# Kernel tuning notes

Hardware: AMD Instinct MI355X
Metric: run time of the kernel (lower is better)

## Reference

```python
import jax, jax.numpy as jnp
import numpy as np

N_NODES = 38000   # 19 feature types x ~2000 categories
IN_DIM = 64
HID = 128         # hid_num in source
R = 8             # number of relations
E = 200000        # edges per relation
N_ROWS = 60000    # data rows
F = 19            # len(features)
N_CLASSES = 10


def setup_inputs() -> dict:
    key = jax.random.key(0)
    ks = jax.random.split(key, 20)
    s_in = 1.0 / np.sqrt(IN_DIM)
    s_h = 1.0 / np.sqrt(HID)
    inp = {
        "node_feats": jax.random.normal(ks[0], (N_NODES, IN_DIM), jnp.float32),
        "edges_src": jax.random.randint(ks[1], (R, E), 0, N_NODES),
        "edges_dst": jax.random.randint(ks[2], (R, E), 0, N_NODES),
        "row_idx": jax.random.randint(ks[3], (N_ROWS, F), 0, N_NODES),
        "row_mask": jax.random.randint(ks[4], (N_ROWS, F), 0, 2).astype(bool),
        # input linear
        "W_in": jax.random.normal(ks[5], (IN_DIM, HID), jnp.float32) * s_in,
        "b_in": jnp.zeros((HID,), jnp.float32),
        # RGCN layer 1 and 2: per-relation GraphConv weights
        "W1": jax.random.normal(ks[6], (R, HID, HID), jnp.float32) * s_h,
        "b1": jnp.zeros((R, HID), jnp.float32),
        "W2": jax.random.normal(ks[7], (R, HID, HID), jnp.float32) * s_h,
        "b2": jnp.zeros((R, HID), jnp.float32),
        # MLP head
        "Wm1": jax.random.normal(ks[8], (HID, HID), jnp.float32) * s_h,
        "bm1": jnp.zeros((HID,), jnp.float32),
        "Wm2": jax.random.normal(ks[9], (HID, HID), jnp.float32) * s_h,
        "bm2": jnp.zeros((HID,), jnp.float32),
        "Wm3": jax.random.normal(ks[10], (HID, N_CLASSES), jnp.float32) * s_h,
        "bm3": jnp.zeros((N_CLASSES,), jnp.float32),
    }
    return inp


def _hetero_conv(h, src, dst, W, b):
    """DGL HeteroGraphConv(sum) of GraphConv(norm='both') over R relations."""
    n = h.shape[0]
    out = jnp.zeros((n, W.shape[2]), h.dtype)
    ones = jnp.ones((src.shape[1],), h.dtype)
    for r in range(src.shape[0]):
        deg_out = jax.ops.segment_sum(ones, src[r], num_segments=n)
        deg_in = jax.ops.segment_sum(ones, dst[r], num_segments=n)
        norm_s = jnp.where(deg_out > 0, deg_out, 1.0) ** -0.5
        norm_d = jnp.where(deg_in > 0, deg_in, 1.0) ** -0.5
        msg = h[src[r]] * norm_s[src[r], None]            # [E, hid]
        agg = jax.ops.segment_sum(msg, dst[r], num_segments=n)
        out = out + (agg * norm_d[:, None]) @ W[r] + b[r]
    return out


def reference(node_feats, edges_src, edges_dst, row_idx, row_mask,
              W_in, b_in, W1, b1, W2, b2, Wm1, bm1, Wm2, bm2, Wm3, bm3):
    # input linear + relu (applied to every node type's features)
    h = jax.nn.relu(node_feats @ W_in + b_in)            # [N_nodes, HID]
    # 2-layer RGCN
    h = jax.nn.relu(_hetero_conv(h, edges_src, edges_dst, W1, b1))
    h = _hetero_conv(h, edges_src, edges_dst, W2, b2)    # [N_nodes, HID]
    # vectorized ragged gather + masked mean (replaces per-row python loop)
    m = row_mask.astype(h.dtype)                          # [N_rows, F]
    emb = h[row_idx] * m[..., None]                       # [N_rows, F, HID]
    cnt = jnp.maximum(m.sum(-1, keepdims=True), 1.0)
    mean_feat = emb.sum(1) / cnt                          # [N_rows, HID]
    # MLP head
    x = jax.nn.relu(mean_feat @ Wm1 + bm1)
    x = jax.nn.relu(x @ Wm2 + bm2)
    return x @ Wm3 + bm3                                  # [N_rows, N_CLASSES]
```

## Files before the change

### kernel.cpp

```cpp
#include <hip/hip_runtime.h>
#include <hip/hip_bf16.h>

#define NN    38000
#define HID   128
#define RR    8
#define EE    200000
#define NROWS 60000
#define FF    19
#define NCLS  10
#define NRD   (RR*NN)
#define HB    38912
#define CH    16
#define CE    (EE/CH)
#define NSEG  19

typedef __hip_bfloat16 bf16;
typedef __attribute__((ext_vector_type(8))) short short8;
typedef __attribute__((ext_vector_type(4))) float floatx4;
typedef __attribute__((ext_vector_type(2))) float float2v;

__device__ __forceinline__ float b2f(bf16 x){ return __bfloat162float(x); }
__device__ __forceinline__ bf16  f2b(float x){ return __float2bfloat16(x); }

__device__ __forceinline__ int geti(const void* a, long long i, int wide){
  return wide ? (int)(((const long long*)a)[i]) : ((const int*)a)[i];
}

__global__ void k_fill(float* out, int n, float v){
  int i = blockIdx.x*256 + threadIdx.x;
  if (i < n) out[i] = v;
}

__global__ void k_sniff(const void* mask, const void* ridx, const void* esrc, int* flags){
  int lane = threadIdx.x;
  const unsigned short* mu = (const unsigned short*)mask;
  int l3f80e=0, l3f80o=0, lbytehi=0, loddnz=0, lother=0;
  for (int i = lane; i < 4096; i += 64){
    unsigned v = mu[i];
    if (v == 0) continue;
    if (v == 0x3F80){ if (i & 1) l3f80o = 1; else l3f80e = 1; continue; }
    unsigned lo = v & 0xFF, hi = v >> 8;
    int lob = (lo == 0 || lo == 1 || lo == 0xFF);
    int hib = (hi == 0 || hi == 1 || hi == 0xFF);
    if (lob && hib){ if (hi) lbytehi = 1; if (i & 1) loddnz = 1; continue; }
    lother = 1;
  }
  int a3f80e = __any(l3f80e);
  int a3f80o = __any(l3f80o);
  int abytehi = __any(lbytehi);
  int aoddnz = __any(loddnz);
  int aother = __any(lother);
  int mtype = -1;
  if (!aother){
    if (a3f80e && !abytehi && !aoddnz)       mtype = 2;
    else if (a3f80o && !a3f80e && !abytehi)  mtype = 3;
    else if (!a3f80e && !a3f80o){
      if (abytehi || aoddnz) mtype = 1;
      else                   mtype = 0;
    }
  }
  const int* es = (const int*)esrc;
  int loddE = 0, lseenE = 0;
  for (int i = lane; i < 512; i += 64){
    if (es[2*i+1] != 0) loddE = 1;
    if (es[2*i] > 1)    lseenE = 1;
  }
  int fE = (!__any(loddE) && __any(lseenE)) ? 1 : 0;
  const int* ri = (const int*)ridx;
  int loddI = 0, lseenI = 0;
  for (int i = lane; i < 512; i += 64){
    if (ri[2*i+1] != 0) loddI = 1;
    if (ri[2*i] > 1)    lseenI = 1;
  }
  int fI = (!__any(loddI) && __any(lseenI)) ? 1 : 0;
  if (lane == 0){ flags[1] = mtype; flags[3] = fE; flags[4] = fI; }
}


__global__ __launch_bounds__(1024) void kg_hist(const void* esrc, const void* edst,
                                                unsigned short* __restrict__ ghd,
                                                unsigned short* __restrict__ ghs,
                                                const int* flags){
  __shared__ int hist[HB];
  int t = threadIdx.x;
  for (int i = t; i < HB; i += 1024) hist[i] = 0;
  __syncthreads();
  int b = blockIdx.x;
  int side = b >> 7;
  int r = (b >> 4) & 7, c = b & 15;
  int wide = flags[3];
  const void* e = side ? esrc : edst;
  long long base = (long long)r*EE + (long long)c*CE;
  if (!wide){
    const int* p = (const int*)e + base;
    for (int i = t; i < CE; i += 1024) atomicAdd(&hist[p[i]], 1);
  } else {
    const long long* p = (const long long*)e + base;
    for (int i = t; i < CE; i += 1024) atomicAdd(&hist[(int)p[i]], 1);
  }
  __syncthreads();
  unsigned short* out = (side ? ghs : ghd) + (long long)(r*CH + c)*HB;
  for (int i = t; i < HB; i += 1024) out[i] = (unsigned short)hist[i];
}

__global__ void kg_tot(const unsigned short* __restrict__ ghd,
                       const unsigned short* __restrict__ ghs,
                       int* __restrict__ totg, float* __restrict__ ns){
  int i = blockIdx.x*256 + threadIdx.x;
  if (i >= RR*HB) return;
  int r = i / HB, bin = i - r*HB;
  int sd = 0, ss = 0;
#pragma unroll
  for (int c = 0; c < CH; c++){
    sd += ghd[(long long)(r*CH+c)*HB + bin];
    ss += ghs[(long long)(r*CH+c)*HB + bin];
  }
  totg[i] = sd;
  if (bin < NN) ns[r*NN + bin] = rsqrtf((float)(ss > 0 ? ss : 1));
}

__global__ __launch_bounds__(1024) void kg_scanA(const int* __restrict__ totg,
                                                 int* __restrict__ rowptr,
                                                 int* __restrict__ segsum){
  __shared__ int wsum[16];
  int b = blockIdx.x;
  int r = b / NSEG, seg = b - r*NSEG;
  int t = threadIdx.x;
  int base = seg*2048;
  int v0 = totg[r*HB + base + 2*t];
  int v1 = totg[r*HB + base + 2*t + 1];
  int s = v0 + v1;
  int lane = t & 63, w = t >> 6;
  int sc = s;
  for (int off = 1; off < 64; off <<= 1){
    int u = __shfl_up(sc, off);
    if (lane >= off) sc += u;
  }
  if (lane == 63) wsum[w] = sc;
  __syncthreads();
  if (t < 16){
    int v = wsum[t];
    int scw = v;
    for (int off = 1; off < 16; off <<= 1){
      int u = __shfl_up(scw, off);
      if (t >= off) scw += u;
    }
    wsum[t] = scw - v;
  }
  __syncthreads();
  int ex = (sc - s) + wsum[w];
  int bin0 = base + 2*t;
  if (bin0 < NN)     rowptr[r*NN + bin0]     = ex;
  if (bin0 + 1 < NN) rowptr[r*NN + bin0 + 1] = ex + v0;
  if (t == 1023) segsum[b] = ex + s;
}

__global__ void kg_scanB(const int* __restrict__ segsum, int* __restrict__ segoff){
  int r = threadIdx.x;
  if (r < RR){
    int acc = r*EE;
    for (int s = 0; s < NSEG; s++){
      int v = segsum[r*NSEG + s];
      segoff[r*NSEG + s] = acc;
      acc += v;
    }
  }
}

__global__ void kg_curs(const unsigned short* __restrict__ ghd,
                        int* __restrict__ rowptr,
                        const int* __restrict__ segoff,
                        int* __restrict__ gcurs){
  int i = blockIdx.x*256 + threadIdx.x;
  if (i >= NRD) return;
  int r = i / NN, bin = i - r*NN;
  int p = rowptr[i] + segoff[r*NSEG + (bin >> 11)];
  rowptr[i] = p;
  if (i == 0) rowptr[NRD] = RR*EE;
#pragma unroll
  for (int c = 0; c < CH; c++){
    gcurs[(long long)(r*CH+c)*HB + bin] = p;
    p += ghd[(long long)(r*CH+c)*HB + bin];
  }
}

__global__ __launch_bounds__(1024) void kg_scatter(const void* esrc, const void* edst,
                                                   const int* __restrict__ gcurs,
                                                   const float* __restrict__ ns,
                                                   int2* __restrict__ csrw, const int* flags){
  __shared__ int cur[HB];
  int t = threadIdx.x, b = blockIdx.x;
  int r = b >> 4, c = b & 15;
  const int* g = gcurs + (long long)(r*CH + c)*HB;
  for (int i = t; i < HB; i += 1024) cur[i] = g[i];
  __syncthreads();
  if (b == 0 && t < 8){ int2 z; z.x = 0; z.y = 0; csrw[RR*EE + t] = z; }
  int wide = flags[3];
  const float* nsr = ns + r*NN;
  long long base = (long long)r*EE + (long long)c*CE;
  if (!wide){
    const int* ps = (const int*)esrc + base;
    const int* pd = (const int*)edst + base;
    for (int i = t; i < CE; i += 1024){
      int d = pd[i], s = ps[i];
      int pos = atomicAdd(&cur[d], 1);
      int2 v; v.x = s << 6; v.y = __float_as_int(nsr[s]);
      csrw[pos] = v;
    }
  } else {
    const long long* ps = (const long long*)esrc + base;
    const long long* pd = (const long long*)edst + base;
    for (int i = t; i < CE; i += 1024){
      int d = (int)pd[i], s = (int)ps[i];
      int pos = atomicAdd(&cur[d], 1);
      int2 v; v.x = s << 6; v.y = __float_as_int(nsr[s]);
      csrw[pos] = v;
    }
  }
}


__global__ void k_packall(const float* __restrict__ W1, const float* __restrict__ W2,
                          const float* __restrict__ Wm1, const float* __restrict__ Wm2,
                          bf16* __restrict__ W1p, bf16* __restrict__ W2p,
                          bf16* __restrict__ Wm1p, bf16* __restrict__ Wm2p,
                          const float* b_in, const float* b1, const float* b2,
                          const float* bm1, const float* bm2, const float* bm3,
                          float* __restrict__ o){
  int idx0 = blockIdx.x*256 + threadIdx.x;
  if (idx0 < 4*65536){
    const float* W = (idx0 < 2*65536) ? W1 : W2;
    bf16* out      = (idx0 < 2*65536) ? W1p : W2p;
    int idx = idx0 & (2*65536 - 1);
    int j = idx & 7;
    int l = (idx >> 3) & 63;
    int t = (idx >> 9) & 127;
    int g = idx >> 16;
    int ktg = t & 15, nt = t >> 4;
    int kglob = ktg*32 + ((l>>4)<<3) + j;
    int rel = kglob >> 7;
    int krow = kglob & 127;
    int n = nt*16 + (l&15);
    out[idx] = f2b(W[((g*4 + rel)*128 + krow)*128 + n]);
  } else if (idx0 < 4*65536 + 2*16384){
    int t2 = idx0 - 4*65536;
    const float* B = (t2 < 16384) ? Wm1 : Wm2;
    bf16* out      = (t2 < 16384) ? Wm1p : Wm2p;
    int idx = t2 & 16383;
    int j  = idx & 7;
    int l  = (idx >> 3) & 63;
    int t  = idx >> 9;
    int kt = t & 3;
    int nt = t >> 2;
    int k = kt*32 + ((l>>4)<<3) + j;
    int n = nt*16 + (l&15);
    out[idx] = f2b(B[k*128 + n]);
  } else if (idx0 < 4*65536 + 2*16384 + 128){
    int t = idx0 - (4*65536 + 2*16384);
    o[t] = b_in[t];
    float s1 = 0.f, s2 = 0.f;
    for (int r = 0; r < RR; r++){ s1 += b1[r*HID+t]; s2 += b2[r*HID+t]; }
    o[128+t] = s1; o[256+t] = s2;
    o[384+t] = bm1[t]; o[512+t] = bm2[t];
    if (t < NCLS) o[640+t] = bm3[t];
  }
}

__global__ void k_gemm_in(const float* __restrict__ A, const float* __restrict__ B,
                          const float* __restrict__ b_in, bf16* __restrict__ out){
  int row0 = blockIdx.x * 4;
  int col = threadIdx.x;
  float a0=0.f, a1=0.f, a2=0.f, a3=0.f;
  for (int k = 0; k < 64; k++){
    float bv = B[k*HID + col];
    a0 += A[(long long)(row0+0)*64 + k] * bv;
    a1 += A[(long long)(row0+1)*64 + k] * bv;
    a2 += A[(long long)(row0+2)*64 + k] * bv;
    a3 += A[(long long)(row0+3)*64 + k] * bv;
  }
  float bb = b_in[col];
  out[(long long)(row0+0)*HID + col] = f2b(fmaxf(a0 + bb, 0.f));
  out[(long long)(row0+1)*HID + col] = f2b(fmaxf(a1 + bb, 0.f));
  out[(long long)(row0+2)*HID + col] = f2b(fmaxf(a2 + bb, 0.f));
  out[(long long)(row0+3)*HID + col] = f2b(fmaxf(a3 + bb, 0.f));
}

#define LOADW(Q, base_) \
  Q##0 = cw[(base_)+0]; Q##1 = cw[(base_)+1]; Q##2 = cw[(base_)+2]; Q##3 = cw[(base_)+3]; \
  Q##4 = cw[(base_)+4]; Q##5 = cw[(base_)+5]; Q##6 = cw[(base_)+6]; Q##7 = cw[(base_)+7];

#define GATHW(P, Q) \
  P##0 = hv[(int)Q##0 + lane]; \
  P##1 = hv[(int)Q##1 + lane]; \
  P##2 = hv[(int)Q##2 + lane]; \
  P##3 = hv[(int)Q##3 + lane]; \
  P##4 = hv[(int)Q##4 + lane]; \
  P##5 = hv[(int)Q##5 + lane]; \
  P##6 = hv[(int)Q##6 + lane]; \
  P##7 = hv[(int)Q##7 + lane];

#define ACCE(Qv, Pv, cond) { \
  float wk_ = (cond) ? __int_as_float((int)((Qv) >> 32)) : 0.f; \
  float2v xv_; \
  xv_.x = __uint_as_float((Pv) << 16); \
  xv_.y = __uint_as_float((Pv) & 0xffff0000u); \
  acc2 += (float2v){wk_, wk_} * xv_; }

#define ROWBODY(i, QC, PC, QN, PN) { \
  int b_ = __builtin_amdgcn_readfirstlane(__shfl(rp, (i))); \
  int e_ = __builtin_amdgcn_readfirstlane(__shfl(rp, (i)+1)); \
  LOADW(QN, e_)                        \
  GATHW(PN, QN)                        \
  float2v acc2 = (float2v){0.f, 0.f}; \
  ACCE(QC##0, PC##0, b_+0 < e_) \
  ACCE(QC##1, PC##1, b_+1 < e_) \
  ACCE(QC##2, PC##2, b_+2 < e_) \
  ACCE(QC##3, PC##3, b_+3 < e_) \
  ACCE(QC##4, PC##4, b_+4 < e_) \
  ACCE(QC##5, PC##5, b_+5 < e_) \
  ACCE(QC##6, PC##6, b_+6 < e_) \
  ACCE(QC##7, PC##7, b_+7 < e_) \
  for (int j = b_ + 8; j < e_; j += 8){       \
    unsigned long long q0 = cw[j],   q1 = cw[j+1], q2 = cw[j+2], q3 = cw[j+3]; \
    unsigned long long q4 = cw[j+4], q5 = cw[j+5], q6 = cw[j+6], q7 = cw[j+7]; \
    unsigned p0 = hv[(int)q0 + lane]; \
    unsigned p1 = hv[(int)q1 + lane]; \
    unsigned p2 = hv[(int)q2 + lane]; \
    unsigned p3 = hv[(int)q3 + lane]; \
    unsigned p4 = hv[(int)q4 + lane]; \
    unsigned p5 = hv[(int)q5 + lane]; \
    unsigned p6 = hv[(int)q6 + lane]; \
    unsigned p7 = hv[(int)q7 + lane]; \
    ACCE(q0, p0, 1) \
    ACCE(q1, p1, j+1 < e_) \
    ACCE(q2, p2, j+2 < e_) \
    ACCE(q3, p3, j+3 < e_) \
    ACCE(q4, p4, j+4 < e_) \
    ACCE(q5, p5, j+5 < e_) \
    ACCE(q6, p6, j+6 < e_) \
    ACCE(q7, p7, j+7 < e_) \
  } \
  int deg = e_ - b_; \
  float nd = rsqrtf((float)(deg > 0 ? deg : 1)); \
  bf16 o0 = f2b(acc2.x * nd), o1 = f2b(acc2.y * nd); \
  unsigned ov = ((unsigned)(*(unsigned short*)&o1) << 16) | (*(unsigned short*)&o0); \
  int addr = (w << 12) + ((i) << 8) + (lane << 2); \
  addr ^= (((i) & 7) << 4); \
  *(unsigned*)(lds + addr) = ov; }

__global__ __launch_bounds__(512) void k_layer(const bf16* __restrict__ h,
                                               const int* __restrict__ rowptr,
                                               const unsigned long long* __restrict__ cw,
                                               const bf16* __restrict__ Bp,
                                               const float* __restrict__ bias,
                                               bf16* __restrict__ hout, int relu){
  __shared__ char lds[8*16*256];
  int w = threadIdx.x >> 6;
  int lane = threadIdx.x & 63;
  int d0 = blockIdx.x << 4;
  const unsigned* hv = (const unsigned*)h;

  int rp = 0;
  if (lane < 17) rp = rowptr[w*NN + d0 + lane];

  unsigned long long qa0,qa1,qa2,qa3,qa4,qa5,qa6,qa7;
  unsigned long long qb0,qb1,qb2,qb3,qb4,qb5,qb6,qb7;
  unsigned pa0,pa1,pa2,pa3,pa4,pa5,pa6,pa7;
  unsigned pb0,pb1,pb2,pb3,pb4,pb5,pb6,pb7;

  {
    int b0_ = __builtin_amdgcn_readfirstlane(__shfl(rp, 0));
    LOADW(qa, b0_)
    GATHW(pa, qa)
  }
  ROWBODY( 0, qa, pa, qb, pb)
  ROWBODY( 1, qb, pb, qa, pa)
  ROWBODY( 2, qa, pa, qb, pb)
  ROWBODY( 3, qb, pb, qa, pa)
  ROWBODY( 4, qa, pa, qb, pb)
  ROWBODY( 5, qb, pb, qa, pa)
  ROWBODY( 6, qa, pa, qb, pb)
  ROWBODY( 7, qb, pb, qa, pa)
  ROWBODY( 8, qa, pa, qb, pb)
  ROWBODY( 9, qb, pb, qa, pa)
  ROWBODY(10, qa, pa, qb, pb)
  ROWBODY(11, qb, pb, qa, pa)
  ROWBODY(12, qa, pa, qb, pb)
  ROWBODY(13, qb, pb, qa, pa)
  ROWBODY(14, qa, pa, qb, pb)
  ROWBODY(15, qb, pb, qa, pa)
  __syncthreads();

  floatx4 acc = (floatx4){0.f,0.f,0.f,0.f};
  int row = lane & 15;
  int kb = (lane >> 4) << 4;
#pragma unroll
  for (int rel = 0; rel < 8; rel++){
    int half = rel >> 2;
    const bf16* bp = Bp + half*65536 + lane*8 + (w*16 + (rel & 3)*4)*512;
#pragma unroll
    for (int ktl = 0; ktl < 4; ktl++){
      int off = (row << 8) + ktl*64 + kb;
      off ^= ((row & 7) << 4);
      short8 a = *(const short8*)(lds + (rel << 12) + off);
      short8 b = *(const short8*)(bp + ktl*512);
      acc = __builtin_amdgcn_mfma_f32_16x16x32_bf16(a, b, acc, 0, 0, 0);
    }
  }
  int col = w*16 + (lane & 15);
  int row0 = d0 + ((lane >> 4) << 2);
  float bb = bias[col];
#pragma unroll
  for (int v = 0; v < 4; v++){
    float x = acc[v] + bb;
    if (relu) x = fmaxf(x, 0.f);
    hout[(long long)(row0 + v)*HID + col] = f2b(x);
  }
}

__global__ __launch_bounds__(256) void k_head(const bf16* __restrict__ h,
                                              const void* ridx, const void* rmask,
                                              const int* __restrict__ flags,
                                              const bf16* __restrict__ Wm1p,
                                              const bf16* __restrict__ Wm2p,
                                              const float* __restrict__ Wm3,
                                              const float* __restrict__ bias,
                                              float* __restrict__ out){
  __shared__ char ldsA[16*256];
  __shared__ char ldsB[16*256];
  int wv = threadIdx.x >> 6;
  int lane = threadIdx.x & 63;
  int r0 = blockIdx.x << 4;
  int mt = flags[1];
  int wide = flags[4];
  const int* m4            = (const int*)rmask;
  const unsigned char* m1  = (const unsigned char*)rmask;
  const unsigned short* m2 = (const unsigned short*)rmask;
  const unsigned int* mw   = (const unsigned int*)rmask;
  const unsigned* hv = (const unsigned*)h;

  for (int rr = 0; rr < 4; rr++){
    int tr = wv*4 + rr;
    int row = r0 + tr;
    int on = 0, idxl = 0;
    if (lane < FF){
      long long i = (long long)row*FF + lane;
      if      (mt == 1) on = (m1[i] != 0);
      else if (mt == 2) on = (m2[i] != 0);
      else if (mt == 3) on = (mw[i] != 0);
      else              on = (m4[i] != 0);
      if (on) idxl = geti(ridx, i, wide);
    }
    unsigned long long bal = __ballot(on);
    float cnt = (float)__popcll(bal);
    float acc0 = 0.f, acc1 = 0.f;
#pragma unroll
    for (int j = 0; j < FF; j++){
      int s = __shfl(idxl, j);
      float wgt = (float)((bal >> j) & 1ull);
      unsigned pv = hv[(long long)s*64 + lane];
      acc0 += wgt * __uint_as_float(pv << 16);
      acc1 += wgt * __uint_as_float(pv & 0xffff0000u);
    }
    float inv = 1.f / fmaxf(cnt, 1.f);
    bf16 o0 = f2b(acc0 * inv), o1 = f2b(acc1 * inv);
    unsigned ov = ((unsigned)(*(unsigned short*)&o1) << 16) | (*(unsigned short*)&o0);
    int addr = (tr << 8) + (lane << 2);
    addr ^= ((tr & 7) << 4);
    *(unsigned*)(ldsA + addr) = ov;
  }
  __syncthreads();

  int arow = lane & 15;
  int kb = (lane >> 4) << 4;
  int colB = lane & 15;
  int rowQ = (lane >> 4) << 2;

  {
    floatx4 accA = (floatx4){0.f,0.f,0.f,0.f};
    floatx4 accB = (floatx4){0.f,0.f,0.f,0.f};
    const bf16* bp = Wm1p + lane*8;
#pragma unroll
    for (int kt = 0; kt < 4; kt++){
      int off = (arow << 8) + kt*64 + kb;
      off ^= ((arow & 7) << 4);
      short8 a = *(const short8*)(ldsA + off);
      short8 b0 = *(const short8*)(bp + ((wv*2+0)*4 + kt)*512);
      short8 b1 = *(const short8*)(bp + ((wv*2+1)*4 + kt)*512);
      accA = __builtin_amdgcn_mfma_f32_16x16x32_bf16(a, b0, accA, 0, 0, 0);
      accB = __builtin_amdgcn_mfma_f32_16x16x32_bf16(a, b1, accB, 0, 0, 0);
    }
#pragma unroll
    for (int ntl = 0; ntl < 2; ntl++){
      int col = (wv*2 + ntl)*16 + colB;
      float bb = bias[384 + col];
#pragma unroll
      for (int v = 0; v < 4; v++){
        float x = ((ntl == 0) ? accA[v] : accB[v]) + bb;
        bf16 xv = f2b(fmaxf(x, 0.f));
        int rowi = rowQ + v;
        int addr = (rowi << 8) + col*2;
        addr ^= ((rowi & 7) << 4);
        *(unsigned short*)(ldsB + addr) = *(unsigned short*)&xv;
      }
    }
  }
  __syncthreads();

  {
    floatx4 accA = (floatx4){0.f,0.f,0.f,0.f};
    floatx4 accB = (floatx4){0.f,0.f,0.f,0.f};
    const bf16* bp = Wm2p + lane*8;
#pragma unroll
    for (int kt = 0; kt < 4; kt++){
      int off = (arow << 8) + kt*64 + kb;
      off ^= ((arow & 7) << 4);
      short8 a = *(const short8*)(ldsB + off);
      short8 b0 = *(const short8*)(bp + ((wv*2+0)*4 + kt)*512);
      short8 b1 = *(const short8*)(bp + ((wv*2+1)*4 + kt)*512);
      accA = __builtin_amdgcn_mfma_f32_16x16x32_bf16(a, b0, accA, 0, 0, 0);
      accB = __builtin_amdgcn_mfma_f32_16x16x32_bf16(a, b1, accB, 0, 0, 0);
    }
#pragma unroll
    for (int ntl = 0; ntl < 2; ntl++){
      int col = (wv*2 + ntl)*16 + colB;
      float bb = bias[512 + col];
#pragma unroll
      for (int v = 0; v < 4; v++){
        float x = ((ntl == 0) ? accA[v] : accB[v]) + bb;
        bf16 xv = f2b(fmaxf(x, 0.f));
        int rowi = rowQ + v;
        int addr = (rowi << 8) + col*2;
        addr ^= ((rowi & 7) << 4);
        *(unsigned short*)(ldsA + addr) = *(unsigned short*)&xv;
      }
    }
  }
  __syncthreads();

  for (int t = threadIdx.x; t < 16*NCLS; t += 256){
    int tr = t / NCLS, col = t - tr*NCLS;
    float acc = bias[640 + col];
    for (int k = 0; k < HID; k++){
      int addr = (tr << 8) + k*2;
      addr ^= ((tr & 7) << 4);
      unsigned short uv = *(const unsigned short*)(ldsA + addr);
      acc += b2f(*(bf16*)&uv) * Wm3[k*NCLS + col];
    }
    out[(long long)(r0 + tr)*NCLS + col] = acc;
  }
}

extern "C" void kernel_launch(void* const* d_in, const int* in_sizes, int n_in,
                              void* d_out, int out_size, void* d_ws, size_t ws_size,
                              hipStream_t stream){
  float* out = (float*)d_out;

  static const int expect[17] = {
    NN*64, RR*EE, RR*EE, NROWS*FF, NROWS*FF,
    64*HID, HID, RR*HID*HID, RR*HID, RR*HID*HID, RR*HID,
    HID*HID, HID, HID*HID, HID, HID*NCLS, NCLS };
  bool ok = (n_in >= 17) && (out_size == NROWS*NCLS);
  if (ok) for (int i = 0; i < 17; i++) if (in_sizes[i] != expect[i]) { ok = false; break; }
  if (!ok){
    k_fill<<<(NROWS*NCLS+255)/256, 256, 0, stream>>>(out, NROWS*NCLS, 64.0f);
    return;
  }

  const void*  e_src = d_in[1];
  const void*  e_dst = d_in[2];
  const void*  ridx  = d_in[3];
  const void*  rmask = d_in[4];
  const float* nf   = (const float*)d_in[0];
  const float* W_in = (const float*)d_in[5];
  const float* b_in = (const float*)d_in[6];
  const float* W1   = (const float*)d_in[7];
  const float* b1   = (const float*)d_in[8];
  const float* W2   = (const float*)d_in[9];
  const float* b2   = (const float*)d_in[10];
  const float* Wm1  = (const float*)d_in[11];
  const float* bm1  = (const float*)d_in[12];
  const float* Wm2  = (const float*)d_in[13];
  const float* bm2  = (const float*)d_in[14];
  const float* Wm3  = (const float*)d_in[15];
  const float* bm3  = (const float*)d_in[16];

  char* ws = (char*)d_ws;
  size_t off = 0;
  auto take = [&](size_t bytes)->char*{
    char* p = ws + off; off += (bytes + 255) & ~(size_t)255; return p; };

  int*   flags  = (int*)  take(256);
  char*  rgn    =         take(58368000);
  unsigned short* ghd = (unsigned short*)(rgn);
  unsigned short* ghs = (unsigned short*)(rgn + 9961472);
  int*   gcurs  = (int*)  (rgn + 19922944);
  int*   totg   = (int*)  (rgn + 39845888);
  int*   segsum = (int*)  (rgn + 41091072);
  int*   segoff = (int*)  (rgn + 41092096);
  bf16*  h1     = (bf16*) take((size_t)NN*HID*2);
  bf16*  h2     = (bf16*) take((size_t)NN*HID*2);
  int*   rowptr = (int*)  take((size_t)(NRD+1)*4);
  int2*  csrw   = (int2*) take((size_t)RR*EE*8 + 64);
  float* ns     = (float*)take((size_t)NRD*4);
  float* bias   = (float*)take(656*4);
  bf16*  W1p    = (bf16*) take((size_t)2*65536*2);
  bf16*  W2p    = (bf16*) take((size_t)2*65536*2);
  bf16*  Wm1p   = (bf16*) take((size_t)16384*2);
  bf16*  Wm2p   = (bf16*) take((size_t)16384*2);

  if (off > ws_size){
    k_fill<<<(NROWS*NCLS+255)/256, 256, 0, stream>>>(out, NROWS*NCLS, 32.0f);
    return;
  }

  k_sniff   <<<1, 64, 0, stream>>>(rmask, ridx, e_src, flags);
  kg_hist   <<<256, 1024, 0, stream>>>(e_src, e_dst, ghd, ghs, flags);
  kg_tot    <<<(RR*HB+255)/256, 256, 0, stream>>>(ghd, ghs, totg, ns);
  kg_scanA  <<<RR*NSEG, 1024, 0, stream>>>(totg, rowptr, segsum);
  kg_scanB  <<<1, 64, 0, stream>>>(segsum, segoff);
  kg_curs   <<<(NRD+255)/256, 256, 0, stream>>>(ghd, rowptr, segoff, gcurs);
  kg_scatter<<<128, 1024, 0, stream>>>(e_src, e_dst, gcurs, ns, csrw, flags);

  k_packall<<<(4*65536 + 2*16384 + 128 + 255)/256, 256, 0, stream>>>(
      W1, W2, Wm1, Wm2, W1p, W2p, Wm1p, Wm2p,
      b_in, b1, b2, bm1, bm2, bm3, bias);

  k_gemm_in<<<NN/4, 128, 0, stream>>>(nf, W_in, b_in, h1);

  k_layer<<<NN/16, 512, 0, stream>>>(h1, rowptr, (const unsigned long long*)csrw,
                                     W1p, bias+128, h2, 1);
  k_layer<<<NN/16, 512, 0, stream>>>(h2, rowptr, (const unsigned long long*)csrw,
                                     W2p, bias+256, h1, 0);

  k_head<<<NROWS/16, 256, 0, stream>>>(h1, ridx, rmask, flags, Wm1p, Wm2p, Wm3, bias, out);
}
```

Baseline: 417.2 us.

## Partition CSR scatter by destination range instead of edge chunks

The scatter is rewritten so that each block owns a range of destination bins for one relation and scans all edges of that relation. Each block seeds its shared-memory cursors straight from rowptr, so the per-chunk cursor array (gcurs) and the pass that wrote it are removed. That saves about 20MB of cursor writes and reads. In exchange, every block now reads all 200k destination indices of its relation (eightfold redundant reads), and the grid shrinks from 128 to 64 blocks, which lowers parallelism.

```diff
diff --git a/kernel.cpp b/kernel.cpp
--- a/kernel.cpp
+++ b/kernel.cpp
@@ -13,6 +13,8 @@
 #define CH    16
 #define CE    (EE/CH)
 #define NSEG  19
+#define RG    8
+#define RGB   (HB/RG)
 
 typedef __hip_bfloat16 bf16;
 typedef __attribute__((ext_vector_type(8))) short short8;
@@ -167,54 +169,57 @@
   }
 }
 
-__global__ void kg_curs(const unsigned short* __restrict__ ghd,
-                        int* __restrict__ rowptr,
-                        const int* __restrict__ segoff,
-                        int* __restrict__ gcurs){
+__global__ void kg_fin(int* __restrict__ rowptr, const int* __restrict__ segoff){
   int i = blockIdx.x*256 + threadIdx.x;
   if (i >= NRD) return;
   int r = i / NN, bin = i - r*NN;
-  int p = rowptr[i] + segoff[r*NSEG + (bin >> 11)];
-  rowptr[i] = p;
+  rowptr[i] += segoff[r*NSEG + (bin >> 11)];
   if (i == 0) rowptr[NRD] = RR*EE;
-#pragma unroll
-  for (int c = 0; c < CH; c++){
-    gcurs[(long long)(r*CH+c)*HB + bin] = p;
-    p += ghd[(long long)(r*CH+c)*HB + bin];
-  }
 }
 
 __global__ __launch_bounds__(1024) void kg_scatter(const void* esrc, const void* edst,
-                                                   const int* __restrict__ gcurs,
+                                                   const int* __restrict__ rowptr,
                                                    const float* __restrict__ ns,
                                                    int2* __restrict__ csrw, const int* flags){
-  __shared__ int cur[HB];
-  int t = threadIdx.x, b = blockIdx.x;
-  int r = b >> 4, c = b & 15;
-  const int* g = gcurs + (long long)(r*CH + c)*HB;
-  for (int i = t; i < HB; i += 1024) cur[i] = g[i];
+  __shared__ int cur[RGB];
+  int b = blockIdx.x;
+  int r = b >> 3, g = b & 7;
+  int lo = g * RGB;
+  int t = threadIdx.x;
+  for (int i = t; i < RGB; i += 1024){
+    int bin = lo + i;
+    cur[i] = (bin < NN) ? rowptr[r*NN + bin] : 0;
+  }
   __syncthreads();
   if (b == 0 && t < 8){ int2 z; z.x = 0; z.y = 0; csrw[RR*EE + t] = z; }
   int wide = flags[3];
   const float* nsr = ns + r*NN;
-  long long base = (long long)r*EE + (long long)c*CE;
+  long long base = (long long)r*EE;
   if (!wide){
     const int* ps = (const int*)esrc + base;
     const int* pd = (const int*)edst + base;
-    for (int i = t; i < CE; i += 1024){
-      int d = pd[i], s = ps[i];
-      int pos = atomicAdd(&cur[d], 1);
-      int2 v; v.x = s << 6; v.y = __float_as_int(nsr[s]);
-      csrw[pos] = v;
+    for (int i = t; i < EE; i += 1024){
+      int d = pd[i];
+      unsigned rd = (unsigned)(d - lo);
+      if (rd < (unsigned)RGB){
+        int s = ps[i];
+        int pos = atomicAdd(&cur[rd], 1);
+        int2 v; v.x = s << 6; v.y = __float_as_int(nsr[s]);
+        csrw[pos] = v;
+      }
     }
   } else {
     const long long* ps = (const long long*)esrc + base;
     const long long* pd = (const long long*)edst + base;
-    for (int i = t; i < CE; i += 1024){
-      int d = (int)pd[i], s = (int)ps[i];
-      int pos = atomicAdd(&cur[d], 1);
-      int2 v; v.x = s << 6; v.y = __float_as_int(nsr[s]);
-      csrw[pos] = v;
+    for (int i = t; i < EE; i += 1024){
+      int d = (int)pd[i];
+      unsigned rd = (unsigned)(d - lo);
+      if (rd < (unsigned)RGB){
+        int s = (int)ps[i];
+        int pos = atomicAdd(&cur[rd], 1);
+        int2 v; v.x = s << 6; v.y = __float_as_int(nsr[s]);
+        csrw[pos] = v;
+      }
     }
   }
 }
@@ -594,10 +599,9 @@
   char*  rgn    =         take(58368000);
   unsigned short* ghd = (unsigned short*)(rgn);
   unsigned short* ghs = (unsigned short*)(rgn + 9961472);
-  int*   gcurs  = (int*)  (rgn + 19922944);
-  int*   totg   = (int*)  (rgn + 39845888);
-  int*   segsum = (int*)  (rgn + 41091072);
-  int*   segoff = (int*)  (rgn + 41092096);
+  int*   totg   = (int*)  (rgn + 19922944);
+  int*   segsum = (int*)  (rgn + 21168128);
+  int*   segoff = (int*)  (rgn + 21169152);
   bf16*  h1     = (bf16*) take((size_t)NN*HID*2);
   bf16*  h2     = (bf16*) take((size_t)NN*HID*2);
   int*   rowptr = (int*)  take((size_t)(NRD+1)*4);
@@ -619,8 +623,8 @@
   kg_tot    <<<(RR*HB+255)/256, 256, 0, stream>>>(ghd, ghs, totg, ns);
   kg_scanA  <<<RR*NSEG, 1024, 0, stream>>>(totg, rowptr, segsum);
   kg_scanB  <<<1, 64, 0, stream>>>(segsum, segoff);
-  kg_curs   <<<(NRD+255)/256, 256, 0, stream>>>(ghd, rowptr, segoff, gcurs);
-  kg_scatter<<<128, 1024, 0, stream>>>(e_src, e_dst, gcurs, ns, csrw, flags);
+  kg_fin    <<<(NRD+255)/256, 256, 0, stream>>>(rowptr, segoff);
+  kg_scatter<<<RR*RG, 1024, 0, stream>>>(e_src, e_dst, rowptr, ns, csrw, flags);
 
   k_packall<<<(4*65536 + 2*16384 + 128 + 255)/256, 256, 0, stream>>>(
       W1, W2, Wm1, Wm2, W1p, W2p, Wm1p, Wm2p,
```

New measurement: 548.2 us. +31.4%, slower.
